# Performance work log

Measured on AMD Instinct MI355X. Metric: run time of the kernel, lower is better.

Reference implementation:

```python
import jax, jax.numpy as jnp
import numpy as np

B, CIN, H, W = 32, 64, 128, 128
HID, OUT, E, S, R = 64, 64, 8, 2, 16
TOP_K = 2
TEMP = 2.0
BN_EPS = 1e-5


def setup_inputs() -> dict:
    key = jax.random.key(0)
    ks = jax.random.split(key, 16)
    sc = lambda fan: 1.0 / np.sqrt(fan)
    h2 = 2 * HID
    return {
        "x": jax.random.normal(ks[0], (B, CIN, H, W), jnp.float32),
        "fe_w": jax.random.normal(ks[1], (HID, CIN), jnp.float32) * sc(CIN),
        "fe_b": jnp.zeros((HID,), jnp.float32),
        "s_w": jax.random.normal(ks[2], (S, OUT, HID), jnp.float32) * sc(HID),
        "s_b": jnp.zeros((S, OUT), jnp.float32),
        "e_w": jax.random.normal(ks[3], (E, OUT, HID), jnp.float32) * sc(HID),
        "e_b": jnp.zeros((E, OUT), jnp.float32),
        "g1_w": jax.random.normal(ks[4], (h2, HID), jnp.float32) * sc(HID),
        "g1_b": jnp.zeros((h2,), jnp.float32),
        "bn1_g": jnp.ones((h2,), jnp.float32),
        "bn1_b": jnp.zeros((h2,), jnp.float32),
        "ca1_w": jax.random.normal(ks[5], (h2 // R, h2), jnp.float32) * sc(h2),
        "ca1_b": jnp.zeros((h2 // R,), jnp.float32),
        "ca2_w": jax.random.normal(ks[6], (h2, h2 // R), jnp.float32) * sc(h2 // R),
        "ca2_b": jnp.zeros((h2,), jnp.float32),
        "g2_w": jax.random.normal(ks[7], (HID, h2), jnp.float32) * sc(h2),
        "g2_b": jnp.zeros((HID,), jnp.float32),
        "bn2_g": jnp.ones((HID,), jnp.float32),
        "bn2_b": jnp.zeros((HID,), jnp.float32),
        "g3_w": jax.random.normal(ks[8], (E, HID), jnp.float32) * sc(HID),
        "g3_b": jnp.zeros((E,), jnp.float32),
    }


def _gelu(v):
    return jax.nn.gelu(v, approximate=False)


def _bn_eval(v, g, b):
    # BatchNorm eval mode with running_mean=0, running_var=1
    return v * (g / np.sqrt(1.0 + BN_EPS)) + b


def reference(x, fe_w, fe_b, s_w, s_b, e_w, e_b, g1_w, g1_b, bn1_g, bn1_b,
              ca1_w, ca1_b, ca2_w, ca2_b, g2_w, g2_b, bn2_g, bn2_b, g3_w, g3_b):
    # feature extractor: 1x1 conv + GELU
    features = _gelu(jnp.einsum('bchw,oc->bohw', x, fe_w) + fe_b[None, :, None, None])

    # shared experts: mean of S expert outputs (sum / S)
    shared = _gelu(jnp.einsum('bchw,soc->bsohw', features, s_w)
                   + s_b[None, :, :, None, None]).mean(axis=1)

    # gating on globally pooled features [B, HID]
    gf = features.mean(axis=(2, 3))
    h1 = _gelu(_bn_eval(gf @ g1_w.T + g1_b, bn1_g, bn1_b))  # [B, 2*HID]
    # ChannelAttention on 1x1 spatial: avg_pool == max_pool == identity
    att = _gelu(h1 @ ca1_w.T + ca1_b) @ ca2_w.T + ca2_b
    h1 = h1 * jax.nn.sigmoid(att + att)  # avg_out + max_out are identical
    hh = _gelu(_bn_eval(h1 @ g2_w.T + g2_b, bn2_g, bn2_b))  # [B, HID]
    scores = hh @ g3_w.T + g3_b  # [B, E]

    top_vals, top_idx = jax.lax.top_k(scores, TOP_K)
    top_w = jax.nn.softmax(top_vals / TEMP, axis=1)  # [B, TOP_K]
    # dense per-(sample, expert) weights
    dense_w = jnp.zeros((x.shape[0], E), scores.dtype).at[
        jnp.arange(x.shape[0])[:, None], top_idx].add(top_w)

    # all experts on full batch, then weighted accumulate (matches original loop)
    eo = _gelu(jnp.einsum('bchw,eoc->beohw', features, e_w)
               + e_b[None, :, :, None, None])  # [B, E, OUT, H, W]
    routed = jnp.einsum('beohw,be->bohw', eo, dense_w)

    return shared + routed
```

## Files before the change

### kernel.cpp

```cpp
#include <hip/hip_runtime.h>
#include <hip/hip_bf16.h>
#include <stdint.h>

#define HW 16384
#define BATCH 32

typedef __bf16 bf16_t;
typedef bf16_t bf16x8 __attribute__((ext_vector_type(8)));
typedef float f32x4 __attribute__((ext_vector_type(4)));

__device__ __forceinline__ float gelu_f(float x) {
    float t = x * fmaf(x * x, 0.044715f, 1.0f);
    float e = __builtin_amdgcn_exp2f(-2.3022083f * t);
    return x * __builtin_amdgcn_rcpf(1.0f + e);
}

__device__ __forceinline__ uint32_t pk2(float a, float b) {
    union { bf16_t h[2]; uint32_t u; } z;
    z.h[0] = (bf16_t)a; z.h[1] = (bf16_t)b;
    return z.u;
}

__device__ __forceinline__ void load16_to_lds(const float* g, float* lds) {
    __builtin_amdgcn_global_load_lds(
        (const __attribute__((address_space(1))) uint32_t*)g,
        (__attribute__((address_space(3))) uint32_t*)lds, 16, 0, 0);
}

__global__ __launch_bounds__(64)
void k0_conv(const float* __restrict__ fe_w, const float* __restrict__ s_w,
             const float* __restrict__ e_w, bf16_t* __restrict__ wbf) {
    int blk = blockIdx.x;
    int m = blk >> 3;
    int ot = (blk >> 1) & 3;
    int kh = blk & 1;
    int lane = threadIdx.x;
    int r16 = lane & 15, g = lane >> 4;

    const float* W;
    if (m == 0) W = fe_w;
    else if (m <= 2) W = s_w + (size_t)(m - 1) * 4096;
    else W = e_w + (size_t)(m - 3) * 4096;

    const float* src = W + (ot * 16 + r16) * 64 + kh * 32 + g * 8;
    float4 lo = ((const float4*)src)[0];
    float4 hi = ((const float4*)src)[1];
    bf16x8 r;
    r[0] = (bf16_t)lo.x; r[1] = (bf16_t)lo.y; r[2] = (bf16_t)lo.z; r[3] = (bf16_t)lo.w;
    r[4] = (bf16_t)hi.x; r[5] = (bf16_t)hi.y; r[6] = (bf16_t)hi.z; r[7] = (bf16_t)hi.w;
    *(bf16x8*)(wbf + (size_t)blk * 512 + lane * 8) = r;
}

__global__ __launch_bounds__(256, 4)
void k1_feat(const float* __restrict__ x, const bf16_t* __restrict__ wbf,
             const float* __restrict__ fe_b, bf16_t* __restrict__ feat,
             float* __restrict__ gf_sum) {
    __shared__ float xs[64 * 128];
    __shared__ float gf4[4][64];

    int tid = threadIdx.x;
    int lane = tid & 63;
    int wid = tid >> 6;
    int r16 = lane & 15;
    int g = lane >> 4;
    int b = blockIdx.x >> 7;
    int stripe = blockIdx.x & 127;
    int p0 = stripe * 128;

    bf16x8 A[4][2];
    f32x4 bias[4];
#pragma unroll
    for (int ot = 0; ot < 4; ++ot) {
#pragma unroll
        for (int kh = 0; kh < 2; ++kh)
            A[ot][kh] = *(const bf16x8*)(wbf + (size_t)(ot * 2 + kh) * 512 + lane * 8);
#pragma unroll
        for (int r = 0; r < 4; ++r) bias[ot][r] = fe_b[ot * 16 + g * 4 + r];
    }

    {
        int rsub = lane >> 5;
        int j = lane & 31;
#pragma unroll
        for (int s = 0; s < 8; ++s) {
            int c = wid * 16 + s * 2 + rsub;
            int gr = (c >> 3) & 3;
            const float* gsrc = x + (size_t)(b * 64 + c) * HW + p0 + ((j ^ (gr << 2)) << 2);
            float* ldst = xs + (wid * 16 + s * 2) * 128;
            load16_to_lds(gsrc, ldst);
        }
    }
    __syncthreads();

    float gfp[4][4] = {};
    bf16_t* featb = feat + (size_t)b * HW * 64;

#pragma unroll
    for (int t = 0; t < 2; ++t) {
        int a = wid * 2 + t;
        int wbase = 16 * (a ^ g) + r16;
        bf16x8 B0, B1;
#pragma unroll
        for (int j = 0; j < 8; ++j) {
            B0[j] = (bf16_t)xs[(g * 8 + j) * 128 + wbase];
            B1[j] = (bf16_t)xs[(32 + g * 8 + j) * 128 + wbase];
        }
        int pg = p0 + a * 16 + r16;
#pragma unroll
        for (int ot = 0; ot < 4; ++ot) {
            f32x4 y = {0.f, 0.f, 0.f, 0.f};
            y = __builtin_amdgcn_mfma_f32_16x16x32_bf16(A[ot][0], B0, y, 0, 0, 0);
            y = __builtin_amdgcn_mfma_f32_16x16x32_bf16(A[ot][1], B1, y, 0, 0, 0);
            float vr[4];
#pragma unroll
            for (int r = 0; r < 4; ++r) {
                float v = gelu_f(y[r] + bias[ot][r]);
                gfp[ot][r] += v;
                vr[r] = v;
            }
            uint2 st;
            st.x = pk2(vr[0], vr[1]);
            st.y = pk2(vr[2], vr[3]);
            *(uint2*)(featb + (size_t)pg * 64 + ot * 16 + g * 4) = st;
        }
    }

#pragma unroll
    for (int ot = 0; ot < 4; ++ot) {
#pragma unroll
        for (int r = 0; r < 4; ++r) {
            float v = gfp[ot][r];
            v += __shfl_xor(v, 1);
            v += __shfl_xor(v, 2);
            v += __shfl_xor(v, 4);
            v += __shfl_xor(v, 8);
            if (r16 == 0) gf4[wid][ot * 16 + g * 4 + r] = v;
        }
    }
    __syncthreads();
    if (tid < 64) {
        float s = gf4[0][tid] + gf4[1][tid] + gf4[2][tid] + gf4[3][tid];
        atomicAdd(gf_sum + b * 64 + tid, s);
    }
}

__global__ __launch_bounds__(256)
void k2_gate(const float* __restrict__ gf_sum,
             const float* __restrict__ g1_w, const float* __restrict__ g1_b,
             const float* __restrict__ bn1_g, const float* __restrict__ bn1_b,
             const float* __restrict__ ca1_w, const float* __restrict__ ca1_b,
             const float* __restrict__ ca2_w, const float* __restrict__ ca2_b,
             const float* __restrict__ g2_w, const float* __restrict__ g2_b,
             const float* __restrict__ bn2_g, const float* __restrict__ bn2_b,
             const float* __restrict__ g3_w, const float* __restrict__ g3_b,
             int* __restrict__ gidx, float* __restrict__ gw) {
    __shared__ float w1t[128 * 65];
    __shared__ float wc1[8 * 129];
    __shared__ float wc2[128 * 9];
    __shared__ float w2t[64 * 129];
    __shared__ float w3[8 * 65];
    __shared__ float gf[64], h1[128], a1[8], hh[64], sc[8];
    const float R1 = 0.99999500003749969f;
    int tid = threadIdx.x;
    int b = blockIdx.x;

    for (int i = tid; i < 2048; i += 256) {
        float4 v = ((const float4*)g1_w)[i];
        float* d = w1t + (i >> 4) * 65 + (i & 15) * 4;
        d[0] = v.x; d[1] = v.y; d[2] = v.z; d[3] = v.w;
    }
    for (int i = tid; i < 2048; i += 256) {
        float4 v = ((const float4*)g2_w)[i];
        float* d = w2t + (i >> 5) * 129 + (i & 31) * 4;
        d[0] = v.x; d[1] = v.y; d[2] = v.z; d[3] = v.w;
    }
    if (tid < 256) {
        int i = tid;
        float4 v = ((const float4*)ca1_w)[i];
        float* d = wc1 + (i >> 5) * 129 + (i & 31) * 4;
        d[0] = v.x; d[1] = v.y; d[2] = v.z; d[3] = v.w;
    }
    if (tid < 256) {
        int i = tid;
        float4 v = ((const float4*)ca2_w)[i];
        float* d = wc2 + (i >> 1) * 9 + (i & 1) * 4;
        d[0] = v.x; d[1] = v.y; d[2] = v.z; d[3] = v.w;
    }
    if (tid < 128) {
        int i = tid;
        float4 v = ((const float4*)g3_w)[i];
        float* d = w3 + (i >> 4) * 65 + (i & 15) * 4;
        d[0] = v.x; d[1] = v.y; d[2] = v.z; d[3] = v.w;
    }
    if (tid < 64) gf[tid] = gf_sum[b * 64 + tid] * (1.0f / 16384.0f);
    __syncthreads();

    if (tid < 128) {
        int j = tid;
        float s = g1_b[j];
#pragma unroll 8
        for (int c = 0; c < 64; ++c) s += gf[c] * w1t[j * 65 + c];
        s = s * (bn1_g[j] * R1) + bn1_b[j];
        h1[j] = gelu_f(s);
    }
    __syncthreads();
    if (tid < 8) {
        int j = tid;
        float s = ca1_b[j];
#pragma unroll 8
        for (int c = 0; c < 128; ++c) s += h1[c] * wc1[j * 129 + c];
        a1[j] = gelu_f(s);
    }
    __syncthreads();
    if (tid < 128) {
        int j = tid;
        float s = ca2_b[j];
#pragma unroll
        for (int r = 0; r < 8; ++r) s += a1[r] * wc2[j * 9 + r];
        float e2 = __builtin_amdgcn_exp2f(-2.8853901f * s);
        h1[j] = h1[j] * __builtin_amdgcn_rcpf(1.0f + e2);
    }
    __syncthreads();
    if (tid < 64) {
        int j = tid;
        float s = g2_b[j];
#pragma unroll 8
        for (int c = 0; c < 128; ++c) s += h1[c] * w2t[j * 129 + c];
        s = s * (bn2_g[j] * R1) + bn2_b[j];
        hh[j] = gelu_f(s);
    }
    __syncthreads();
    if (tid < 8) {
        int j = tid;
        float s = g3_b[j];
#pragma unroll 8
        for (int c = 0; c < 64; ++c) s += hh[c] * w3[j * 65 + c];
        sc[j] = s;
    }
    __syncthreads();
    if (tid == 0) {
        float v0 = -1e30f, v1 = -1e30f;
        int i0 = 0, i1 = 0;
#pragma unroll
        for (int e = 0; e < 8; ++e) {
            float s = sc[e];
            if (s > v0) { v1 = v0; i1 = i0; v0 = s; i0 = e; }
            else if (s > v1) { v1 = s; i1 = e; }
        }
        float t = __builtin_amdgcn_exp2f(0.7213475f * (v1 - v0));
        float den = __builtin_amdgcn_rcpf(1.0f + t);
        gidx[b * 2] = i0; gidx[b * 2 + 1] = i1;
        gw[b * 2] = den; gw[b * 2 + 1] = t * den;
    }
}

__global__ __launch_bounds__(256, 4)
void k3_out(const bf16_t* __restrict__ feat, const bf16_t* __restrict__ wbf,
            const float* __restrict__ s_b, const float* __restrict__ e_b,
            const int* __restrict__ gidx, const float* __restrict__ gw,
            float* __restrict__ out) {
    int tid = threadIdx.x;
    int lane = tid & 63, wid = tid >> 6;
    int r16 = lane & 15, g = lane >> 4;
    int b = blockIdx.x >> 5;
    int stripe = blockIdx.x & 31;

    int i0 = gidx[2 * b], i1 = gidx[2 * b + 1];
    float coef[4] = {0.5f, 0.5f, gw[2 * b], gw[2 * b + 1]};
    int mats[4] = {1, 2, 3 + i0, 3 + i1};
    const float* Bm[4] = {s_b, s_b + 64, e_b + i0 * 64, e_b + i1 * 64};

    bf16x8 A[4][2];
    f32x4 biasr[4];
#pragma unroll
    for (int m = 0; m < 4; ++m) {
#pragma unroll
        for (int kh = 0; kh < 2; ++kh)
            A[m][kh] = *(const bf16x8*)(wbf + (size_t)((mats[m] * 4 + wid) * 2 + kh) * 512 + lane * 8);
#pragma unroll
        for (int r = 0; r < 4; ++r) biasr[m][r] = Bm[m][wid * 16 + g * 4 + r];
    }

    const uint4* fb = (const uint4*)(feat + (size_t)b * HW * 64);
    float* outb = out + (size_t)b * 64 * HW + (size_t)(wid * 16 + g * 4) * HW;
    int pbase = stripe * 512 + r16;

#pragma unroll 2
    for (int t = 0; t < 32; ++t) {
        int p = pbase + t * 16;
        uint4 u0 = fb[p * 8 + g];
        uint4 u1 = fb[p * 8 + 4 + g];
        bf16x8 B0 = __builtin_bit_cast(bf16x8, u0);
        bf16x8 B1 = __builtin_bit_cast(bf16x8, u1);
        f32x4 acc = {0.f, 0.f, 0.f, 0.f};
#pragma unroll
        for (int m = 0; m < 4; ++m) {
            f32x4 y = {0.f, 0.f, 0.f, 0.f};
            y = __builtin_amdgcn_mfma_f32_16x16x32_bf16(A[m][0], B0, y, 0, 0, 0);
            y = __builtin_amdgcn_mfma_f32_16x16x32_bf16(A[m][1], B1, y, 0, 0, 0);
#pragma unroll
            for (int r = 0; r < 4; ++r)
                acc[r] += coef[m] * gelu_f(y[r] + biasr[m][r]);
        }
#pragma unroll
        for (int r = 0; r < 4; ++r)
            outb[(size_t)r * HW + p] = acc[r];
    }
}

extern "C" void kernel_launch(void* const* d_in, const int* in_sizes, int n_in,
                              void* d_out, int out_size, void* d_ws, size_t ws_size,
                              hipStream_t stream) {
    const float* x     = (const float*)d_in[0];
    const float* fe_w  = (const float*)d_in[1];
    const float* fe_b  = (const float*)d_in[2];
    const float* s_w   = (const float*)d_in[3];
    const float* s_b   = (const float*)d_in[4];
    const float* e_w   = (const float*)d_in[5];
    const float* e_b   = (const float*)d_in[6];
    const float* g1_w  = (const float*)d_in[7];
    const float* g1_b  = (const float*)d_in[8];
    const float* bn1_g = (const float*)d_in[9];
    const float* bn1_b = (const float*)d_in[10];
    const float* ca1_w = (const float*)d_in[11];
    const float* ca1_b = (const float*)d_in[12];
    const float* ca2_w = (const float*)d_in[13];
    const float* ca2_b = (const float*)d_in[14];
    const float* g2_w  = (const float*)d_in[15];
    const float* g2_b  = (const float*)d_in[16];
    const float* bn2_g = (const float*)d_in[17];
    const float* bn2_b = (const float*)d_in[18];
    const float* g3_w  = (const float*)d_in[19];
    const float* g3_b  = (const float*)d_in[20];
    float* out = (float*)d_out;

    char* wsb = (char*)d_ws;
    bf16_t* feat  = (bf16_t*)wsb;
    float* gf_sum = (float*)(wsb + (size_t)67108864);
    int* gidx     = (int*)(wsb + 67108864 + 8192);
    float* gwts   = (float*)(wsb + 67108864 + 8192 + 256);
    bf16_t* wbf   = (bf16_t*)(wsb + 67125248);

    hipMemsetAsync(gf_sum, 0, 32 * 64 * sizeof(float), stream);
    k0_conv<<<88, 64, 0, stream>>>(fe_w, s_w, e_w, wbf);
    k1_feat<<<4096, 256, 0, stream>>>(x, wbf, fe_b, feat, gf_sum);
    k2_gate<<<32, 256, 0, stream>>>(gf_sum, g1_w, g1_b, bn1_g, bn1_b, ca1_w, ca1_b,
                                    ca2_w, ca2_b, g2_w, g2_b, bn2_g, bn2_b, g3_w, g3_b,
                                    gidx, gwts);
    k3_out<<<1024, 256, 0, stream>>>(feat, wbf, s_b, e_b, gidx, gwts, out);
}
```

Baseline: 338.0 us.

## Pipeline feature conv with double-buffered LDS, drop weight-convert kernel and atomics

The feature kernel now runs 1024 blocks, each covering 512 pixels, and double-buffers the x tiles in LDS with asynchronous loads overlapping compute. The separate weight-conversion kernel and the memset are removed: weights are converted to bf16 inside each kernel, and pooled sums are written as per-block partials instead of atomics. The output kernel swaps the MFMA operand order so each lane writes contiguous float4s, and it prefetches the next feature fragment. The gate kernel splits its dot products into two accumulators. The cost is redundant weight conversion in every block and more manual waitcnt and barrier handling, which must be exactly right.

New measurement: 388.5 us. +14.9%, slower.

```diff
diff --git a/kernel.cpp b/kernel.cpp
--- a/kernel.cpp
+++ b/kernel.cpp
@@ -3,7 +3,6 @@
 #include <stdint.h>
 
 #define HW 16384
-#define BATCH 32
 
 typedef __bf16 bf16_t;
 typedef bf16_t bf16x8 __attribute__((ext_vector_type(8)));
@@ -27,35 +26,20 @@
         (__attribute__((address_space(3))) uint32_t*)lds, 16, 0, 0);
 }
 
-__global__ __launch_bounds__(64)
-void k0_conv(const float* __restrict__ fe_w, const float* __restrict__ s_w,
-             const float* __restrict__ e_w, bf16_t* __restrict__ wbf) {
-    int blk = blockIdx.x;
-    int m = blk >> 3;
-    int ot = (blk >> 1) & 3;
-    int kh = blk & 1;
-    int lane = threadIdx.x;
-    int r16 = lane & 15, g = lane >> 4;
-
-    const float* W;
-    if (m == 0) W = fe_w;
-    else if (m <= 2) W = s_w + (size_t)(m - 1) * 4096;
-    else W = e_w + (size_t)(m - 3) * 4096;
-
-    const float* src = W + (ot * 16 + r16) * 64 + kh * 32 + g * 8;
+__device__ __forceinline__ bf16x8 frag8(const float* src) {
     float4 lo = ((const float4*)src)[0];
     float4 hi = ((const float4*)src)[1];
     bf16x8 r;
     r[0] = (bf16_t)lo.x; r[1] = (bf16_t)lo.y; r[2] = (bf16_t)lo.z; r[3] = (bf16_t)lo.w;
     r[4] = (bf16_t)hi.x; r[5] = (bf16_t)hi.y; r[6] = (bf16_t)hi.z; r[7] = (bf16_t)hi.w;
-    *(bf16x8*)(wbf + (size_t)blk * 512 + lane * 8) = r;
+    return r;
 }
 
 __global__ __launch_bounds__(256, 4)
-void k1_feat(const float* __restrict__ x, const bf16_t* __restrict__ wbf,
+void k1_feat(const float* __restrict__ x, const float* __restrict__ fe_w,
              const float* __restrict__ fe_b, bf16_t* __restrict__ feat,
-             float* __restrict__ gf_sum) {
-    __shared__ float xs[64 * 128];
+             float* __restrict__ gf_part) {
+    __shared__ float xs[2][64 * 64];
     __shared__ float gf4[4][64];
 
     int tid = threadIdx.x;
@@ -63,9 +47,9 @@
     int wid = tid >> 6;
     int r16 = lane & 15;
     int g = lane >> 4;
-    int b = blockIdx.x >> 7;
-    int stripe = blockIdx.x & 127;
-    int p0 = stripe * 128;
+    int b = blockIdx.x >> 5;
+    int ss = blockIdx.x & 31;
+    int p0 = ss * 512;
 
     bf16x8 A[4][2];
     f32x4 bias[4];
@@ -73,39 +57,37 @@
     for (int ot = 0; ot < 4; ++ot) {
 #pragma unroll
         for (int kh = 0; kh < 2; ++kh)
-            A[ot][kh] = *(const bf16x8*)(wbf + (size_t)(ot * 2 + kh) * 512 + lane * 8);
+            A[ot][kh] = frag8(fe_w + (ot * 16 + r16) * 64 + kh * 32 + g * 8);
 #pragma unroll
         for (int r = 0; r < 4; ++r) bias[ot][r] = fe_b[ot * 16 + g * 4 + r];
     }
 
-    {
-        int rsub = lane >> 5;
-        int j = lane & 31;
-#pragma unroll
-        for (int s = 0; s < 8; ++s) {
-            int c = wid * 16 + s * 2 + rsub;
-            int gr = (c >> 3) & 3;
-            const float* gsrc = x + (size_t)(b * 64 + c) * HW + p0 + ((j ^ (gr << 2)) << 2);
-            float* ldst = xs + (wid * 16 + s * 2) * 128;
-            load16_to_lds(gsrc, ldst);
-        }
-    }
-    __syncthreads();
+    int j16 = lane & 15;
+    int rsub = lane >> 4;
+
+    auto STAGE = [&](int buf, int i) {
+#pragma unroll
+        for (int s = 0; s < 4; ++s) {
+            int c0 = wid * 16 + s * 4;
+            int c = c0 + rsub;
+            int gch = j16 ^ (((c >> 3) & 3) << 2);
+            const float* gsrc = x + (size_t)(b * 64 + c) * HW + p0 + i * 64 + gch * 4;
+            load16_to_lds(gsrc, &xs[buf][c0 * 64]);
+        }
+    };
 
     float gfp[4][4] = {};
     bf16_t* featb = feat + (size_t)b * HW * 64;
-
-#pragma unroll
-    for (int t = 0; t < 2; ++t) {
-        int a = wid * 2 + t;
-        int wbase = 16 * (a ^ g) + r16;
+    int wb = 16 * (wid ^ g) + r16;
+
+    auto COMPUTE = [&](int buf, int i) {
         bf16x8 B0, B1;
 #pragma unroll
         for (int j = 0; j < 8; ++j) {
-            B0[j] = (bf16_t)xs[(g * 8 + j) * 128 + wbase];
-            B1[j] = (bf16_t)xs[(32 + g * 8 + j) * 128 + wbase];
-        }
-        int pg = p0 + a * 16 + r16;
+            B0[j] = (bf16_t)xs[buf][(g * 8 + j) * 64 + wb];
+            B1[j] = (bf16_t)xs[buf][(32 + g * 8 + j) * 64 + wb];
+        }
+        int pg = p0 + i * 64 + wid * 16 + r16;
 #pragma unroll
         for (int ot = 0; ot < 4; ++ot) {
             f32x4 y = {0.f, 0.f, 0.f, 0.f};
@@ -123,10 +105,30 @@
             st.y = pk2(vr[2], vr[3]);
             *(uint2*)(featb + (size_t)pg * 64 + ot * 16 + g * 4) = st;
         }
-    }
-
-#pragma unroll
-    for (int ot = 0; ot < 4; ++ot) {
+    };
+
+    STAGE(0, 0);
+    STAGE(1, 1);
+    asm volatile("s_waitcnt vmcnt(4)" ::: "memory");
+    __builtin_amdgcn_s_barrier();
+
+#pragma unroll
+    for (int i = 0; i < 8; ++i) {
+        COMPUTE(i & 1, i);
+        asm volatile("s_waitcnt lgkmcnt(0)" ::: "memory");
+        __builtin_amdgcn_s_barrier();
+        if (i < 6) {
+            STAGE(i & 1, i + 2);
+            asm volatile("s_waitcnt vmcnt(8)" ::: "memory");
+            __builtin_amdgcn_s_barrier();
+        } else if (i == 6) {
+            asm volatile("s_waitcnt vmcnt(4)" ::: "memory");
+            __builtin_amdgcn_s_barrier();
+        }
+    }
+
+#pragma unroll
+    for (int ot = 0; ot < 4; ++ot)
 #pragma unroll
         for (int r = 0; r < 4; ++r) {
             float v = gfp[ot][r];
@@ -136,16 +138,14 @@
             v += __shfl_xor(v, 8);
             if (r16 == 0) gf4[wid][ot * 16 + g * 4 + r] = v;
         }
-    }
-    __syncthreads();
-    if (tid < 64) {
-        float s = gf4[0][tid] + gf4[1][tid] + gf4[2][tid] + gf4[3][tid];
-        atomicAdd(gf_sum + b * 64 + tid, s);
-    }
+    __syncthreads();
+    if (tid < 64)
+        gf_part[(size_t)blockIdx.x * 64 + tid] =
+            gf4[0][tid] + gf4[1][tid] + gf4[2][tid] + gf4[3][tid];
 }
 
 __global__ __launch_bounds__(256)
-void k2_gate(const float* __restrict__ gf_sum,
+void k2_gate(const float* __restrict__ gf_part,
              const float* __restrict__ g1_w, const float* __restrict__ g1_b,
              const float* __restrict__ bn1_g, const float* __restrict__ bn1_b,
              const float* __restrict__ ca1_w, const float* __restrict__ ca1_b,
@@ -192,24 +192,39 @@
         float* d = w3 + (i >> 4) * 65 + (i & 15) * 4;
         d[0] = v.x; d[1] = v.y; d[2] = v.z; d[3] = v.w;
     }
-    if (tid < 64) gf[tid] = gf_sum[b * 64 + tid] * (1.0f / 16384.0f);
+    if (tid < 64) {
+        float s0 = 0.f, s1 = 0.f;
+#pragma unroll
+        for (int ssi = 0; ssi < 32; ssi += 2) {
+            s0 += gf_part[(size_t)(b * 32 + ssi) * 64 + tid];
+            s1 += gf_part[(size_t)(b * 32 + ssi + 1) * 64 + tid];
+        }
+        gf[tid] = (s0 + s1) * (1.0f / 16384.0f);
+    }
     __syncthreads();
 
     if (tid < 128) {
         int j = tid;
-        float s = g1_b[j];
+        float s0 = 0.f, s1 = 0.f;
 #pragma unroll 8
-        for (int c = 0; c < 64; ++c) s += gf[c] * w1t[j * 65 + c];
+        for (int c = 0; c < 64; c += 2) {
+            s0 += gf[c] * w1t[j * 65 + c];
+            s1 += gf[c + 1] * w1t[j * 65 + c + 1];
+        }
+        float s = g1_b[j] + s0 + s1;
         s = s * (bn1_g[j] * R1) + bn1_b[j];
         h1[j] = gelu_f(s);
     }
     __syncthreads();
     if (tid < 8) {
         int j = tid;
-        float s = ca1_b[j];
+        float s0 = 0.f, s1 = 0.f;
 #pragma unroll 8
-        for (int c = 0; c < 128; ++c) s += h1[c] * wc1[j * 129 + c];
-        a1[j] = gelu_f(s);
+        for (int c = 0; c < 128; c += 2) {
+            s0 += h1[c] * wc1[j * 129 + c];
+            s1 += h1[c + 1] * wc1[j * 129 + c + 1];
+        }
+        a1[j] = gelu_f(ca1_b[j] + s0 + s1);
     }
     __syncthreads();
     if (tid < 128) {
@@ -223,19 +238,26 @@
     __syncthreads();
     if (tid < 64) {
         int j = tid;
-        float s = g2_b[j];
+        float s0 = 0.f, s1 = 0.f;
 #pragma unroll 8
-        for (int c = 0; c < 128; ++c) s += h1[c] * w2t[j * 129 + c];
+        for (int c = 0; c < 128; c += 2) {
+            s0 += h1[c] * w2t[j * 129 + c];
+            s1 += h1[c + 1] * w2t[j * 129 + c + 1];
+        }
+        float s = g2_b[j] + s0 + s1;
         s = s * (bn2_g[j] * R1) + bn2_b[j];
         hh[j] = gelu_f(s);
     }
     __syncthreads();
     if (tid < 8) {
         int j = tid;
-        float s = g3_b[j];
+        float s0 = 0.f, s1 = 0.f;
 #pragma unroll 8
-        for (int c = 0; c < 64; ++c) s += hh[c] * w3[j * 65 + c];
-        sc[j] = s;
+        for (int c = 0; c < 64; c += 2) {
+            s0 += hh[c] * w3[j * 65 + c];
+            s1 += hh[c + 1] * w3[j * 65 + c + 1];
+        }
+        sc[j] = g3_b[j] + s0 + s1;
     }
     __syncthreads();
     if (tid == 0) {
@@ -255,10 +277,10 @@
 }
 
 __global__ __launch_bounds__(256, 4)
-void k3_out(const bf16_t* __restrict__ feat, const bf16_t* __restrict__ wbf,
-            const float* __restrict__ s_b, const float* __restrict__ e_b,
-            const int* __restrict__ gidx, const float* __restrict__ gw,
-            float* __restrict__ out) {
+void k3_out(const bf16_t* __restrict__ feat, const float* __restrict__ s_w,
+            const float* __restrict__ s_b, const float* __restrict__ e_w,
+            const float* __restrict__ e_b, const int* __restrict__ gidx,
+            const float* __restrict__ gw, float* __restrict__ out) {
     int tid = threadIdx.x;
     int lane = tid & 63, wid = tid >> 6;
     int r16 = lane & 15, g = lane >> 4;
@@ -267,50 +289,58 @@
 
     int i0 = gidx[2 * b], i1 = gidx[2 * b + 1];
     float coef[4] = {0.5f, 0.5f, gw[2 * b], gw[2 * b + 1]};
-    int mats[4] = {1, 2, 3 + i0, 3 + i1};
-    const float* Bm[4] = {s_b, s_b + 64, e_b + i0 * 64, e_b + i1 * 64};
-
-    bf16x8 A[4][2];
-    f32x4 biasr[4];
+    const float* Wm[4] = {s_w, s_w + 4096,
+                          e_w + (size_t)i0 * 4096, e_w + (size_t)i1 * 4096};
+    const float* Bv[4] = {s_b, s_b + 64, e_b + i0 * 64, e_b + i1 * 64};
+
+    bf16x8 Wf[4][2];
+    float bias[4];
+    int row = wid * 16 + r16;
 #pragma unroll
     for (int m = 0; m < 4; ++m) {
 #pragma unroll
         for (int kh = 0; kh < 2; ++kh)
-            A[m][kh] = *(const bf16x8*)(wbf + (size_t)((mats[m] * 4 + wid) * 2 + kh) * 512 + lane * 8);
-#pragma unroll
-        for (int r = 0; r < 4; ++r) biasr[m][r] = Bm[m][wid * 16 + g * 4 + r];
+            Wf[m][kh] = frag8(Wm[m] + row * 64 + kh * 32 + g * 8);
+        bias[m] = Bv[m][row];
     }
 
     const uint4* fb = (const uint4*)(feat + (size_t)b * HW * 64);
-    float* outb = out + (size_t)b * 64 * HW + (size_t)(wid * 16 + g * 4) * HW;
+    float* outb = out + ((size_t)b * 64 + row) * HW + stripe * 512;
     int pbase = stripe * 512 + r16;
 
-#pragma unroll 2
-    for (int t = 0; t < 32; ++t) {
-        int p = pbase + t * 16;
-        uint4 u0 = fb[p * 8 + g];
-        uint4 u1 = fb[p * 8 + 4 + g];
-        bf16x8 B0 = __builtin_bit_cast(bf16x8, u0);
-        bf16x8 B1 = __builtin_bit_cast(bf16x8, u1);
+    auto BODY = [&](int t, uint4 u0, uint4 u1) {
+        bf16x8 F0 = __builtin_bit_cast(bf16x8, u0);
+        bf16x8 F1 = __builtin_bit_cast(bf16x8, u1);
         f32x4 acc = {0.f, 0.f, 0.f, 0.f};
 #pragma unroll
         for (int m = 0; m < 4; ++m) {
             f32x4 y = {0.f, 0.f, 0.f, 0.f};
-            y = __builtin_amdgcn_mfma_f32_16x16x32_bf16(A[m][0], B0, y, 0, 0, 0);
-            y = __builtin_amdgcn_mfma_f32_16x16x32_bf16(A[m][1], B1, y, 0, 0, 0);
+            y = __builtin_amdgcn_mfma_f32_16x16x32_bf16(F0, Wf[m][0], y, 0, 0, 0);
+            y = __builtin_amdgcn_mfma_f32_16x16x32_bf16(F1, Wf[m][1], y, 0, 0, 0);
 #pragma unroll
             for (int r = 0; r < 4; ++r)
-                acc[r] += coef[m] * gelu_f(y[r] + biasr[m][r]);
-        }
-#pragma unroll
-        for (int r = 0; r < 4; ++r)
-            outb[(size_t)r * HW + p] = acc[r];
-    }
+                acc[r] += coef[m] * gelu_f(y[r] + bias[m]);
+        }
+        float4 st = {acc[0], acc[1], acc[2], acc[3]};
+        *(float4*)(outb + t * 16 + g * 4) = st;
+    };
+
+    uint4 u0 = fb[(size_t)pbase * 8 + g];
+    uint4 u1 = fb[(size_t)pbase * 8 + 4 + g];
+#pragma unroll 4
+    for (int t = 0; t < 31; ++t) {
+        uint4 n0 = fb[(size_t)(pbase + (t + 1) * 16) * 8 + g];
+        uint4 n1 = fb[(size_t)(pbase + (t + 1) * 16) * 8 + 4 + g];
+        BODY(t, u0, u1);
+        u0 = n0; u1 = n1;
+    }
+    BODY(31, u0, u1);
 }
 
 extern "C" void kernel_launch(void* const* d_in, const int* in_sizes, int n_in,
                               void* d_out, int out_size, void* d_ws, size_t ws_size,
                               hipStream_t stream) {
+    (void)in_sizes; (void)n_in; (void)out_size; (void)ws_size;
     const float* x     = (const float*)d_in[0];
     const float* fe_w  = (const float*)d_in[1];
     const float* fe_b  = (const float*)d_in[2];
@@ -335,17 +365,14 @@
     float* out = (float*)d_out;
 
     char* wsb = (char*)d_ws;
-    bf16_t* feat  = (bf16_t*)wsb;
-    float* gf_sum = (float*)(wsb + (size_t)67108864);
-    int* gidx     = (int*)(wsb + 67108864 + 8192);
-    float* gwts   = (float*)(wsb + 67108864 + 8192 + 256);
-    bf16_t* wbf   = (bf16_t*)(wsb + 67125248);
-
-    hipMemsetAsync(gf_sum, 0, 32 * 64 * sizeof(float), stream);
-    k0_conv<<<88, 64, 0, stream>>>(fe_w, s_w, e_w, wbf);
-    k1_feat<<<4096, 256, 0, stream>>>(x, wbf, fe_b, feat, gf_sum);
-    k2_gate<<<32, 256, 0, stream>>>(gf_sum, g1_w, g1_b, bn1_g, bn1_b, ca1_w, ca1_b,
+    bf16_t* feat   = (bf16_t*)wsb;
+    float* gf_part = (float*)(wsb + 67108864);
+    int* gidx      = (int*)(wsb + 67108864 + 262144);
+    float* gwts    = (float*)(wsb + 67108864 + 262144 + 256);
+
+    k1_feat<<<1024, 256, 0, stream>>>(x, fe_w, fe_b, feat, gf_part);
+    k2_gate<<<32, 256, 0, stream>>>(gf_part, g1_w, g1_b, bn1_g, bn1_b, ca1_w, ca1_b,
                                     ca2_w, ca2_b, g2_w, g2_b, bn2_g, bn2_b, g3_w, g3_b,
                                     gidx, gwts);
-    k3_out<<<1024, 256, 0, stream>>>(feat, wbf, s_b, e_b, gidx, gwts, out);
-}
+    k3_out<<<1024, 256, 0, stream>>>(feat, s_w, s_b, e_w, e_b, gidx, gwts, out);
+}
```
